# Kernel optimization log

Measured on AMD Instinct MI355X. Metric: run time of the kernel, lower is better.

The kernel has to match this reference:

```python
import jax, jax.numpy as jnp
import numpy as np

N_NODES = 100000
N_EDGES = 1600000
N_FEAT = 128
HIDDEN = 64
N_CLASSES = 16


def setup_inputs() -> dict:
    key = jax.random.key(0)
    ks = jax.random.split(key, 8)
    x = jax.random.normal(ks[0], (N_NODES, N_FEAT), dtype=jnp.float32)
    edge_index = jax.random.randint(ks[1], (2, N_EDGES), 0, N_NODES, dtype=jnp.int64)
    def glorot(k, shape):
        lim = float(np.sqrt(6.0 / (shape[0] + shape[1])))
        return jax.random.uniform(k, shape, jnp.float32, -lim, lim)
    return {
        "x": x,
        "edge_index": edge_index,
        "W0": glorot(ks[2], (N_FEAT, HIDDEN)), "b0": jnp.zeros((HIDDEN,), jnp.float32),
        "W1": glorot(ks[3], (HIDDEN, HIDDEN)), "b1": jnp.zeros((HIDDEN,), jnp.float32),
        "W2": glorot(ks[4], (HIDDEN, 2)),      "b2": jnp.zeros((2,), jnp.float32),
        "Wc": glorot(ks[5], (2, N_CLASSES)),   "bc": jnp.zeros((N_CLASSES,), jnp.float32),
    }


def _gcn_conv(x, W, b, src, dst, norm, n_nodes):
    # GCNConv: D^{-1/2} (A + I) D^{-1/2} X W + b, edges already include self-loops
    h = x @ W                                  # transform first (small dim)
    msg = h[src] * norm[:, None]               # gather + per-edge scale
    agg = jax.ops.segment_sum(msg, dst, num_segments=n_nodes)  # scatter-add
    return agg + b


def reference(x, edge_index, W0, b0, W1, b1, W2, b2, Wc, bc):
    n = x.shape[0]
    loops = jnp.arange(n, dtype=edge_index.dtype)
    src = jnp.concatenate([edge_index[0], loops])
    dst = jnp.concatenate([edge_index[1], loops])
    # degree on destination (col), including self-loops
    deg = jax.ops.segment_sum(jnp.ones_like(dst, dtype=x.dtype), dst, num_segments=n)
    dis = jnp.where(deg > 0, jax.lax.rsqrt(deg), 0.0)
    norm = dis[src] * dis[dst]

    h = _gcn_conv(x, W0, b0, src, dst, norm, n)              # layer 0, no activation
    h = jnp.tanh(_gcn_conv(h, W1, b1, src, dst, norm, n))    # layer 1
    h = jnp.tanh(_gcn_conv(h, W2, b2, src, dst, norm, n))    # layer 2 -> [N, 2]
    embeddings = h
    out = embeddings @ Wc + bc                               # [N, num_classes]
    return (out, embeddings)
```

## Files before the change

### kernel.cpp

```cpp
#include <hip/hip_runtime.h>


#define NF 128
#define NH 64
#define NPB 256
#define MAXNB 512
#define CAP 6144
#define A1G 1024

typedef _Float16 half8 __attribute__((ext_vector_type(8)));
typedef float f32x4 __attribute__((ext_vector_type(4)));

__global__ void k_init0(const int* __restrict__ ei, int* __restrict__ fmt,
                        int* __restrict__ ccnt, int nb16) {
    int i = blockIdx.x * 256 + threadIdx.x;
    if (i < nb16) ccnt[i] = 0;
    if (i == 0) {
        int f = 1;
        #pragma unroll
        for (int k = 1; k < 32; k += 2) if (ei[k] != 0) f = 0;
        *fmt = f;
    }
}

__global__ void __launch_bounds__(256) k_coarse(
        const int* __restrict__ ei, const int* __restrict__ fmt,
        int* __restrict__ ccnt, int* __restrict__ blockbase, int E, int NB) {
    __shared__ int h[MAXNB];
    int sh = *fmt;
    for (int i = threadIdx.x; i < NB; i += 256) h[i] = 0;
    __syncthreads();
    for (long long e = (long long)blockIdx.x * 256 + threadIdx.x; e < E;
         e += (long long)A1G * 256) {
        int d = ei[(long long)(E + e) << sh];
        atomicAdd(&h[d >> 8], 1);
    }
    __syncthreads();
    for (int b = threadIdx.x; b < NB; b += 256) {
        int c = h[b];
        int base = (c > 0) ? atomicAdd(&ccnt[b * 16], c) : 0;
        blockbase[(long long)blockIdx.x * NB + b] = base;
    }
}

__global__ void __launch_bounds__(512) k_cscan(
        const int* __restrict__ ccnt, int* __restrict__ cstart, int NB) {
    __shared__ int s[512];
    int t = threadIdx.x;
    int c = (t < NB) ? ccnt[t * 16] : 0;
    s[t] = c;
    __syncthreads();
    for (int off = 1; off < 512; off <<= 1) {
        int v = s[t];
        int u = (t >= off) ? s[t - off] : 0;
        __syncthreads();
        s[t] = v + u;
        __syncthreads();
    }
    if (t < NB) cstart[t] = s[t] - c;
}

__global__ void __launch_bounds__(256) k_cscatter(
        const int* __restrict__ ei, const int* __restrict__ fmt,
        const int* __restrict__ cstart, const int* __restrict__ blockbase,
        int* __restrict__ pairs, int E, int NB) {
    __shared__ int h[MAXNB];
    __shared__ int bb[MAXNB];
    int sh = *fmt;
    for (int i = threadIdx.x; i < NB; i += 256) {
        h[i] = 0;
        bb[i] = cstart[i] + blockbase[(long long)blockIdx.x * NB + i];
    }
    __syncthreads();
    for (long long e = (long long)blockIdx.x * 256 + threadIdx.x; e < E;
         e += (long long)A1G * 256) {
        int s = ei[(long long)e << sh];
        int d = ei[(long long)(E + e) << sh];
        int b = d >> 8;
        int r = atomicAdd(&h[b], 1);
        pairs[bb[b] + r] = s | ((d & 255) << 17);
    }
}

__global__ void __launch_bounds__(256) k_bucket(
        const int* __restrict__ pairs, const int* __restrict__ ccnt,
        const int* __restrict__ cstart, int* __restrict__ esrc,
        int* __restrict__ cnt, int* __restrict__ start, float* __restrict__ dis,
        int N) {
    __shared__ int words[CAP];
    __shared__ unsigned char rk[CAP];
    __shared__ int h[NPB];
    __shared__ int hs[NPB];
    int b = blockIdx.x;
    int cs = cstart[b];
    int ec = ccnt[b * 16];
    if (ec > CAP) ec = CAP;
    int t = threadIdx.x;
    for (int i = t; i < ec; i += 256) words[i] = pairs[cs + i];
    h[t] = 0;
    __syncthreads();
    for (int i = t; i < ec; i += 256) {
        int ld = words[i] >> 17;
        rk[i] = (unsigned char)atomicAdd(&h[ld], 1);
    }
    __syncthreads();
    int c = h[t];
    hs[t] = c;
    __syncthreads();
    for (int off = 1; off < 256; off <<= 1) {
        int v = hs[t];
        int u = (t >= off) ? hs[t - off] : 0;
        __syncthreads();
        hs[t] = v + u;
        __syncthreads();
    }
    int node = b * NPB + t;
    if (node < N) {
        cnt[node] = c;
        start[node] = cs + hs[t] - c;
        dis[node] = rsqrtf(1.0f + (float)c);
    }
    for (int i = t; i < ec; i += 256) {
        int w = words[i];
        int ld = w >> 17;
        esrc[cs + (hs[ld] - h[ld]) + rk[i]] = w & 0x1FFFF;
    }
}

__global__ void k_wprep(const float* __restrict__ W0, const float* __restrict__ W1,
                        short* __restrict__ wf0, short* __restrict__ wf1) {
    int b = blockIdx.x;
    int t = threadIdx.x;
    int lane = t & 63;
    int j0 = (t >> 6) * 2;
    const float* W = (b < 16) ? W0 : W1;
    int bb = (b < 16) ? b : (b - 16);
    short* wf = (b < 16) ? wf0 : wf1;
    int lohalf = (b < 16) ? 8192 : 4096;
    int kc = bb >> 2, ct = bb & 3;
    #pragma unroll
    for (int jj = 0; jj < 2; ++jj) {
        int j = j0 + jj;
        int k = kc * 32 + (lane >> 4) * 8 + j;
        int col = ct * 16 + (lane & 15);
        float w = W[k * NH + col];
        _Float16 h = (_Float16)w;
        _Float16 l = (_Float16)(w - (float)h);
        int idx = (bb * 64 + lane) * 8 + j;
        wf[idx] = *(short*)&h;
        wf[idx + lohalf] = *(short*)&l;
    }
}

#define GEMM_EPILOGUE                                                         \
    int rb = (int)rowbase + wid * 16 + (lane >> 4) * 4;                       \
    float drs[4];                                                             \
    drs[0] = (rb + 0 < n) ? dis[rb + 0] : 0.0f;                               \
    drs[1] = (rb + 1 < n) ? dis[rb + 1] : 0.0f;                               \
    drs[2] = (rb + 2 < n) ? dis[rb + 2] : 0.0f;                               \
    drs[3] = (rb + 3 < n) ? dis[rb + 3] : 0.0f;                               \
    const float ks = 1.0f / 32767.0f;                                         \
    int cb = lane & 15;                                                       \
    _Pragma("unroll")                                                         \
    for (int r = 0; r < 4; ++r) {                                             \
        float v0 = acc0[r] * drs[r];                                          \
        float v1 = acc1[r] * drs[r];                                          \
        float v2 = acc2[r] * drs[r];                                          \
        float v3 = acc3[r] * drs[r];                                          \
        float m = fmaxf(fmaxf(fabsf(v0), fabsf(v1)), fmaxf(fabsf(v2), fabsf(v3))); \
        m = fmaxf(m, __shfl_xor(m, 1, 64));                                   \
        m = fmaxf(m, __shfl_xor(m, 2, 64));                                   \
        m = fmaxf(m, __shfl_xor(m, 4, 64));                                   \
        m = fmaxf(m, __shfl_xor(m, 8, 64));                                   \
        float ir = 32767.0f / fmaxf(m, 1e-20f);                               \
        int rowg = rb + r;                                                    \
        if (rowg < n) {                                                       \
            long long base = (long long)rowg * NH;                            \
            T16[base + 0  + cb] = (short)__float2int_rn(v0 * ir);             \
            T16[base + 16 + cb] = (short)__float2int_rn(v1 * ir);             \
            T16[base + 32 + cb] = (short)__float2int_rn(v2 * ir);             \
            T16[base + 48 + cb] = (short)__float2int_rn(v3 * ir);             \
            if (cb == 0) rs[rowg] = m * ks;                                   \
        }                                                                     \
    }

#define CVT_AFRAG(xa, xb4)                                                    \
    half8 ah, al;                                                             \
    {                                                                         \
        float xv[8] = {xa.x, xa.y, xa.z, xa.w, xb4.x, xb4.y, xb4.z, xb4.w};   \
        _Pragma("unroll")                                                     \
        for (int e = 0; e < 8; ++e) {                                         \
            _Float16 h = (_Float16)xv[e];                                     \
            ah[e] = h;                                                        \
            al[e] = (_Float16)(xv[e] - (float)h);                             \
        }                                                                     \
    }

#define MFMA3(ACC, SETIDX, LOHALF)                                            \
    {                                                                         \
        const half8 bh = *(const half8*)&Wf[((SETIDX) * 64 + lane) * 8];      \
        const half8 bl = *(const half8*)&Wf[((SETIDX) * 64 + lane) * 8 + (LOHALF)]; \
        ACC = __builtin_amdgcn_mfma_f32_16x16x32_f16(ah, bh, ACC, 0, 0, 0);   \
        ACC = __builtin_amdgcn_mfma_f32_16x16x32_f16(ah, bl, ACC, 0, 0, 0);   \
        ACC = __builtin_amdgcn_mfma_f32_16x16x32_f16(al, bh, ACC, 0, 0, 0);   \
    }

__global__ void __launch_bounds__(256) k_gemmM(
        const float* __restrict__ X, const short* __restrict__ wfrag,
        const float* __restrict__ dis, short* __restrict__ T16,
        float* __restrict__ rs, int n) {
    __shared__ __align__(16) short Wf[16384];
    int tid = threadIdx.x;
    {
        const int4* src = (const int4*)wfrag;
        int4* dst = (int4*)Wf;
        #pragma unroll
        for (int u = 0; u < 8; ++u) dst[tid + u * 256] = src[tid + u * 256];
    }
    __syncthreads();
    long long rowbase = (long long)blockIdx.x * 64;
    int lane = tid & 63;
    int wid = tid >> 6;
    int row = (int)rowbase + wid * 16 + (lane & 15);
    bool ok = row < n;
    const float* xb = X + (long long)row * NF + (lane >> 4) * 8;
    f32x4 acc0 = {0,0,0,0}, acc1 = {0,0,0,0}, acc2 = {0,0,0,0}, acc3 = {0,0,0,0};
    #pragma unroll
    for (int kc = 0; kc < 4; ++kc) {
        float4 xa = ok ? *(const float4*)(xb + kc * 32)
                       : make_float4(0.f, 0.f, 0.f, 0.f);
        float4 xc = ok ? *(const float4*)(xb + kc * 32 + 4)
                       : make_float4(0.f, 0.f, 0.f, 0.f);
        CVT_AFRAG(xa, xc)
        MFMA3(acc0, kc * 4 + 0, 8192)
        MFMA3(acc1, kc * 4 + 1, 8192)
        MFMA3(acc2, kc * 4 + 2, 8192)
        MFMA3(acc3, kc * 4 + 3, 8192)
    }
    GEMM_EPILOGUE
}

__global__ void __launch_bounds__(256) k_gemmM64(
        const float* __restrict__ H, const short* __restrict__ wfrag,
        const float* __restrict__ dis, short* __restrict__ T16,
        float* __restrict__ rs, int n) {
    __shared__ __align__(16) short Wf[8192];
    int tid = threadIdx.x;
    {
        const int4* src = (const int4*)wfrag;
        int4* dst = (int4*)Wf;
        #pragma unroll
        for (int u = 0; u < 4; ++u) dst[tid + u * 256] = src[tid + u * 256];
    }
    __syncthreads();
    long long rowbase = (long long)blockIdx.x * 64;
    int lane = tid & 63;
    int wid = tid >> 6;
    int row = (int)rowbase + wid * 16 + (lane & 15);
    bool ok = row < n;
    const float* hb = H + (long long)row * NH + (lane >> 4) * 8;
    f32x4 acc0 = {0,0,0,0}, acc1 = {0,0,0,0}, acc2 = {0,0,0,0}, acc3 = {0,0,0,0};
    #pragma unroll
    for (int kc = 0; kc < 2; ++kc) {
        float4 xa = ok ? *(const float4*)(hb + kc * 32)
                       : make_float4(0.f, 0.f, 0.f, 0.f);
        float4 xc = ok ? *(const float4*)(hb + kc * 32 + 4)
                       : make_float4(0.f, 0.f, 0.f, 0.f);
        CVT_AFRAG(xa, xc)
        MFMA3(acc0, kc * 4 + 0, 4096)
        MFMA3(acc1, kc * 4 + 1, 4096)
        MFMA3(acc2, kc * 4 + 2, 4096)
        MFMA3(acc3, kc * 4 + 3, 4096)
    }
    GEMM_EPILOGUE
}

#define EDGE_A(J) {                                                           \
    int s_ = __builtin_amdgcn_readlane(sA, (J));                              \
    float f_ = __int_as_float(__builtin_amdgcn_readlane(fAb, (J)));           \
    accA = fmaf(f_, (float)(T + s_ * NH)[lane], accA); }
#define EDGE_B(J) {                                                           \
    int s_ = __builtin_amdgcn_readlane(sB, (J));                              \
    float f_ = __int_as_float(__builtin_amdgcn_readlane(fBb, (J)));           \
    accB = fmaf(f_, (float)(T + s_ * NH)[lane], accB); }

#define SEG_GATHER2                                                           \
    int lane = threadIdx.x & 63;                                              \
    int na = blockIdx.x * 8 + (threadIdx.x >> 6) * 2;                         \
    int nb_ = na + 1;                                                         \
    if (na >= n) return;                                                      \
    bool hasB = (nb_ < n);                                                    \
    float dia = dis[na];                                                      \
    float dib = hasB ? dis[nb_] : 0.0f;                                       \
    int ga = cnt[na], sta = start[na];                                        \
    int gb = hasB ? cnt[nb_] : 0;                                             \
    int stb = hasB ? start[nb_] : 0;                                          \
    float accA = rs[na] * (float)T[na * NH + lane];                           \
    float accB = hasB ? rs[nb_] * (float)T[nb_ * NH + lane] : 0.0f;           \
    int gmax = ga > gb ? ga : gb;                                             \
    for (int base = 0; base < gmax; base += 64) {                             \
        int ma = ga - base; ma = ma < 0 ? 0 : (ma > 64 ? 64 : ma);            \
        int mb = gb - base; mb = mb < 0 ? 0 : (mb > 64 ? 64 : mb);            \
        int sA = 0, sB = 0; float fA = 0.0f, fB = 0.0f;                       \
        if (lane < ma) { sA = esrc[sta + base + lane]; fA = rs[sA]; }         \
        if (lane < mb) { sB = esrc[stb + base + lane]; fB = rs[sB]; }         \
        int fAb = __float_as_int(fA), fBb = __float_as_int(fB);               \
        int mmin = ma < mb ? ma : mb;                                         \
        int j = 0;                                                            \
        for (; j + 3 < mmin; j += 4) {                                        \
            EDGE_A(j + 0) EDGE_B(j + 0)                                       \
            EDGE_A(j + 1) EDGE_B(j + 1)                                       \
            EDGE_A(j + 2) EDGE_B(j + 2)                                       \
            EDGE_A(j + 3) EDGE_B(j + 3)                                       \
        }                                                                     \
        int jA = j, jB = j;                                                   \
        for (; jA + 3 < ma; jA += 4) {                                        \
            EDGE_A(jA + 0) EDGE_A(jA + 1) EDGE_A(jA + 2) EDGE_A(jA + 3)       \
        }                                                                     \
        for (; jA < ma; ++jA) EDGE_A(jA)                                      \
        for (; jB + 3 < mb; jB += 4) {                                        \
            EDGE_B(jB + 0) EDGE_B(jB + 1) EDGE_B(jB + 2) EDGE_B(jB + 3)       \
        }                                                                     \
        for (; jB < mb; ++jB) EDGE_B(jB)                                      \
    }

__global__ void __launch_bounds__(256) k_seg(
        const short* __restrict__ T, const float* __restrict__ rs,
        const int* __restrict__ esrc, const int* __restrict__ start,
        const int* __restrict__ cnt, const float* __restrict__ dis,
        const float* __restrict__ b0, float* __restrict__ O, int n) {
    SEG_GATHER2
    float bv = b0[lane];
    O[(long long)na * NH + lane] = dia * accA + bv;
    if (hasB) O[(long long)nb_ * NH + lane] = dib * accB + bv;
}

__global__ void __launch_bounds__(256) k_seg1f(
        const short* __restrict__ T, const float* __restrict__ rs,
        const int* __restrict__ esrc, const int* __restrict__ start,
        const int* __restrict__ cnt, const float* __restrict__ dis,
        const float* __restrict__ b1, const float* __restrict__ W2,
        float2* __restrict__ t2, int n) {
    SEG_GATHER2
    float bv = b1[lane];
    float2 w = ((const float2*)W2)[lane];
    float tA = tanhf(dia * accA + bv);
    float p0 = tA * w.x, p1 = tA * w.y;
    float tB = hasB ? tanhf(dib * accB + bv) : 0.0f;
    float q0 = tB * w.x, q1 = tB * w.y;
    #pragma unroll
    for (int msk = 32; msk; msk >>= 1) {
        p0 += __shfl_xor(p0, msk, 64);
        p1 += __shfl_xor(p1, msk, 64);
        q0 += __shfl_xor(q0, msk, 64);
        q1 += __shfl_xor(q1, msk, 64);
    }
    if (lane == 0) {
        t2[na] = make_float2(dia * p0, dia * p1);
        if (hasB) t2[nb_] = make_float2(dib * q0, dib * q1);
    }
}

__global__ void __launch_bounds__(256) k_seg2f(
        const float2* __restrict__ T2, const int* __restrict__ esrc,
        const int* __restrict__ start, const int* __restrict__ cnt,
        const float* __restrict__ dis, const float* __restrict__ b2,
        const float* __restrict__ Wc, const float* __restrict__ bc,
        float* __restrict__ out, float* __restrict__ emb, int n) {
    int lane = threadIdx.x & 63;
    int sub = lane >> 4;
    int sl = lane & 15;
    int i = blockIdx.x * 16 + (threadIdx.x >> 6) * 4 + sub;
    if (i >= n) return;
    float di = dis[i];
    int g = cnt[i], st = start[i];
    float a0 = 0.0f, a1 = 0.0f;
    for (int j = sl; j < g; j += 16) {
        float2 v = T2[esrc[st + j]];
        a0 += v.x; a1 += v.y;
    }
    if (sl == 0) {
        float2 s = T2[i];
        a0 += s.x; a1 += s.y;
    }
    #pragma unroll
    for (int msk = 8; msk; msk >>= 1) {
        a0 += __shfl_xor(a0, msk, 64);
        a1 += __shfl_xor(a1, msk, 64);
    }
    float e0 = tanhf(a0 * di + b2[0]);
    float e1 = tanhf(a1 * di + b2[1]);
    if (sl == 0) *(float2*)&emb[(long long)i * 2] = make_float2(e0, e1);
    if (sl < 4) {
        int c = sl * 4;
        float4 o;
        o.x = e0 * Wc[c + 0] + e1 * Wc[16 + c + 0] + bc[c + 0];
        o.y = e0 * Wc[c + 1] + e1 * Wc[16 + c + 1] + bc[c + 1];
        o.z = e0 * Wc[c + 2] + e1 * Wc[16 + c + 2] + bc[c + 2];
        o.w = e0 * Wc[c + 3] + e1 * Wc[16 + c + 3] + bc[c + 3];
        *(float4*)&out[(long long)i * 16 + c] = o;
    }
}

extern "C" void kernel_launch(void* const* d_in, const int* in_sizes, int n_in,
                              void* d_out, int out_size, void* d_ws, size_t ws_size,
                              hipStream_t stream) {
    const float* x  = (const float*)d_in[0];
    const int*   ei = (const int*)  d_in[1];
    const float* W0 = (const float*)d_in[2];
    const float* b0 = (const float*)d_in[3];
    const float* W1 = (const float*)d_in[4];
    const float* b1 = (const float*)d_in[5];
    const float* W2 = (const float*)d_in[6];
    const float* b2 = (const float*)d_in[7];
    const float* Wc = (const float*)d_in[8];
    const float* bc = (const float*)d_in[9];

    int N = in_sizes[0] / NF;
    int E = in_sizes[1] / 2;
    int NB = (N + NPB - 1) / NPB;

    float* out = (float*)d_out;
    float* emb = out + (long long)N * 16;

    short*  T16a = (short*)d_ws;
    float*  Bb   = (float*)((char*)d_ws + (long long)N * NH * 2);
    float*  dis  = (float*)((char*)d_ws + (long long)N * NH * 2 + (long long)N * NH * 4);
    float*  rs_a = dis + N;
    int*    cnt   = (int*)(rs_a + N);
    int*    start = cnt + N;
    int*    esrc  = start + N;
    int*    fmt   = esrc + E;
    short*  wf0   = (short*)d_out;
    short*  wf1   = wf0 + 16384;
    float2* t2    = (float2*)Bb;

    int* pairs     = (int*)d_ws;
    int* blockbase = pairs + E;
    int* ccnt      = blockbase + (long long)A1G * NB;
    int* cstart    = ccnt + NB * 16;

    int nb_g  = (N + 63) / 64;
    int nb_s2 = (N + 7) / 8;
    int nb_2f = (N + 15) / 16;
    int nb_i0 = (NB * 16 + 255) / 256;

    k_wprep   <<<24, 256, 0, stream>>>(W0, W1, wf0, wf1);

    k_init0   <<<nb_i0, 256, 0, stream>>>(ei, fmt, ccnt, NB * 16);
    k_coarse  <<<A1G, 256, 0, stream>>>(ei, fmt, ccnt, blockbase, E, NB);
    k_cscan   <<<1, 512, 0, stream>>>(ccnt, cstart, NB);
    k_cscatter<<<A1G, 256, 0, stream>>>(ei, fmt, cstart, blockbase, pairs, E, NB);
    k_bucket  <<<NB, 256, 0, stream>>>(pairs, ccnt, cstart, esrc, cnt, start, dis, N);

    k_gemmM   <<<nb_g, 256, 0, stream>>>(x, wf0, dis, T16a, rs_a, N);

    k_seg     <<<nb_s2, 256, 0, stream>>>(T16a, rs_a, esrc, start, cnt, dis, b0,
                                          Bb, N);

    k_gemmM64 <<<nb_g, 256, 0, stream>>>(Bb, wf1, dis, T16a, rs_a, N);

    k_seg1f   <<<nb_s2, 256, 0, stream>>>(T16a, rs_a, esrc, start, cnt, dis, b1,
                                          W2, t2, N);

    k_seg2f   <<<nb_2f, 256, 0, stream>>>(t2, esrc, start, cnt, dis, b2, Wc, bc,
                                          out, emb, N);
}
```

Baseline: 303.6 us.

## Merge weight prep into init kernel, halve coarse-sort grid and unroll edge loops

Merges the weight-splitting kernel and the counter-init kernel into one launch, removing one kernel launch. Halves the grid of the coarse histogram and scatter kernels, which shrinks the per-block blockbase array and its initialisation traffic. The edge loops are unrolled by four so several index loads are in flight before the shared-memory atomics. Fewer blocks means each block handles more edges, which may lower parallelism in these passes.

```diff
diff --git a/kernel.cpp b/kernel.cpp
--- a/kernel.cpp
+++ b/kernel.cpp
@@ -6,14 +6,40 @@
 #define NPB 256
 #define MAXNB 512
 #define CAP 6144
-#define A1G 1024
+#define A1G 512
 
 typedef _Float16 half8 __attribute__((ext_vector_type(8)));
 typedef float f32x4 __attribute__((ext_vector_type(4)));
 
-__global__ void k_init0(const int* __restrict__ ei, int* __restrict__ fmt,
+__global__ void k_prep0(const float* __restrict__ W0, const float* __restrict__ W1,
+                        short* __restrict__ wf0, short* __restrict__ wf1,
+                        const int* __restrict__ ei, int* __restrict__ fmt,
                         int* __restrict__ ccnt, int nb16) {
-    int i = blockIdx.x * 256 + threadIdx.x;
+    int b = blockIdx.x;
+    int t = threadIdx.x;
+    if (b < 24) {
+        int lane = t & 63;
+        int j0 = (t >> 6) * 2;
+        const float* W = (b < 16) ? W0 : W1;
+        int bb = (b < 16) ? b : (b - 16);
+        short* wf = (b < 16) ? wf0 : wf1;
+        int lohalf = (b < 16) ? 8192 : 4096;
+        int kc = bb >> 2, ct = bb & 3;
+        #pragma unroll
+        for (int jj = 0; jj < 2; ++jj) {
+            int j = j0 + jj;
+            int k = kc * 32 + (lane >> 4) * 8 + j;
+            int col = ct * 16 + (lane & 15);
+            float w = W[k * NH + col];
+            _Float16 h = (_Float16)w;
+            _Float16 l = (_Float16)(w - (float)h);
+            int idx = (bb * 64 + lane) * 8 + j;
+            wf[idx] = *(short*)&h;
+            wf[idx + lohalf] = *(short*)&l;
+        }
+        return;
+    }
+    int i = (b - 24) * 256 + t;
     if (i < nb16) ccnt[i] = 0;
     if (i == 0) {
         int f = 1;
@@ -30,8 +56,19 @@
     int sh = *fmt;
     for (int i = threadIdx.x; i < NB; i += 256) h[i] = 0;
     __syncthreads();
-    for (long long e = (long long)blockIdx.x * 256 + threadIdx.x; e < E;
-         e += (long long)A1G * 256) {
+    const long long S = (long long)A1G * 256;
+    long long e = (long long)blockIdx.x * 256 + threadIdx.x;
+    for (; e + 3 * S < E; e += 4 * S) {
+        int d0 = ei[(long long)(E + e) << sh];
+        int d1 = ei[(long long)(E + e + S) << sh];
+        int d2 = ei[(long long)(E + e + 2 * S) << sh];
+        int d3 = ei[(long long)(E + e + 3 * S) << sh];
+        atomicAdd(&h[d0 >> 8], 1);
+        atomicAdd(&h[d1 >> 8], 1);
+        atomicAdd(&h[d2 >> 8], 1);
+        atomicAdd(&h[d3 >> 8], 1);
+    }
+    for (; e < E; e += S) {
         int d = ei[(long long)(E + e) << sh];
         atomicAdd(&h[d >> 8], 1);
     }
@@ -72,8 +109,28 @@
         bb[i] = cstart[i] + blockbase[(long long)blockIdx.x * NB + i];
     }
     __syncthreads();
-    for (long long e = (long long)blockIdx.x * 256 + threadIdx.x; e < E;
-         e += (long long)A1G * 256) {
+    const long long S = (long long)A1G * 256;
+    long long e = (long long)blockIdx.x * 256 + threadIdx.x;
+    for (; e + 3 * S < E; e += 4 * S) {
+        int s0 = ei[(long long)e << sh];
+        int s1 = ei[(long long)(e + S) << sh];
+        int s2 = ei[(long long)(e + 2 * S) << sh];
+        int s3 = ei[(long long)(e + 3 * S) << sh];
+        int d0 = ei[(long long)(E + e) << sh];
+        int d1 = ei[(long long)(E + e + S) << sh];
+        int d2 = ei[(long long)(E + e + 2 * S) << sh];
+        int d3 = ei[(long long)(E + e + 3 * S) << sh];
+        int b0 = d0 >> 8, b1 = d1 >> 8, b2 = d2 >> 8, b3 = d3 >> 8;
+        int r0 = atomicAdd(&h[b0], 1);
+        pairs[bb[b0] + r0] = s0 | ((d0 & 255) << 17);
+        int r1 = atomicAdd(&h[b1], 1);
+        pairs[bb[b1] + r1] = s1 | ((d1 & 255) << 17);
+        int r2 = atomicAdd(&h[b2], 1);
+        pairs[bb[b2] + r2] = s2 | ((d2 & 255) << 17);
+        int r3 = atomicAdd(&h[b3], 1);
+        pairs[bb[b3] + r3] = s3 | ((d3 & 255) << 17);
+    }
+    for (; e < E; e += S) {
         int s = ei[(long long)e << sh];
         int d = ei[(long long)(E + e) << sh];
         int b = d >> 8;
@@ -124,31 +181,6 @@
         int w = words[i];
         int ld = w >> 17;
         esrc[cs + (hs[ld] - h[ld]) + rk[i]] = w & 0x1FFFF;
-    }
-}
-
-__global__ void k_wprep(const float* __restrict__ W0, const float* __restrict__ W1,
-                        short* __restrict__ wf0, short* __restrict__ wf1) {
-    int b = blockIdx.x;
-    int t = threadIdx.x;
-    int lane = t & 63;
-    int j0 = (t >> 6) * 2;
-    const float* W = (b < 16) ? W0 : W1;
-    int bb = (b < 16) ? b : (b - 16);
-    short* wf = (b < 16) ? wf0 : wf1;
-    int lohalf = (b < 16) ? 8192 : 4096;
-    int kc = bb >> 2, ct = bb & 3;
-    #pragma unroll
-    for (int jj = 0; jj < 2; ++jj) {
-        int j = j0 + jj;
-        int k = kc * 32 + (lane >> 4) * 8 + j;
-        int col = ct * 16 + (lane & 15);
-        float w = W[k * NH + col];
-        _Float16 h = (_Float16)w;
-        _Float16 l = (_Float16)(w - (float)h);
-        int idx = (bb * 64 + lane) * 8 + j;
-        wf[idx] = *(short*)&h;
-        wf[idx + lohalf] = *(short*)&l;
     }
 }
 
@@ -443,11 +475,11 @@
     int nb_g  = (N + 63) / 64;
     int nb_s2 = (N + 7) / 8;
     int nb_2f = (N + 15) / 16;
-    int nb_i0 = (NB * 16 + 255) / 256;
-
-    k_wprep   <<<24, 256, 0, stream>>>(W0, W1, wf0, wf1);
-
-    k_init0   <<<nb_i0, 256, 0, stream>>>(ei, fmt, ccnt, NB * 16);
+    int nb16  = NB * 16;
+    int nb_i0 = (nb16 + 255) / 256;
+
+    k_prep0   <<<24 + nb_i0, 256, 0, stream>>>(W0, W1, wf0, wf1, ei, fmt,
+                                               ccnt, nb16);
     k_coarse  <<<A1G, 256, 0, stream>>>(ei, fmt, ccnt, blockbase, E, NB);
     k_cscan   <<<1, 512, 0, stream>>>(ccnt, cstart, NB);
     k_cscatter<<<A1G, 256, 0, stream>>>(ei, fmt, cstart, blockbase, pairs, E, NB);
```

After: 277.4 us, median of 2. 8.6% less time.
